# Performance work log

Measured on AMD Instinct MI355X. Metric: run time of the kernel, lower is better.

## Reference

```python
import jax, jax.numpy as jnp
import numpy as np

B, N, C, H = 4, 2048, 768, 12
D = C // H  # head_dim = 64


def setup_inputs() -> dict:
    key = jax.random.key(0)
    ks = jax.random.split(key, 16)
    s = 1.0 / np.sqrt(C)
    inp = {
        "x1": jax.random.normal(ks[0], (B, N, C), jnp.float32),
        "x2": jax.random.normal(ks[1], (B, N, C), jnp.float32),
        "mask_1": jax.random.uniform(ks[2], (B, N), jnp.float32),
        "mask_2": jax.random.uniform(ks[3], (B, N), jnp.float32),
        "Wq": jax.random.normal(ks[4], (C, C), jnp.float32) * s,
        "bq": jnp.zeros((C,), jnp.float32),
        "Wk": jax.random.normal(ks[5], (C, C), jnp.float32) * s,
        "bk": jnp.zeros((C,), jnp.float32),
        "Wv": jax.random.normal(ks[6], (C, C), jnp.float32) * s,
        "bv": jnp.zeros((C,), jnp.float32),
        "Wo": jax.random.normal(ks[7], (C, C), jnp.float32) * s,
        "bo": jnp.zeros((C,), jnp.float32),
        "temperature": jnp.asarray(1.0, jnp.float32),
        "ln_gamma": jnp.ones((C,), jnp.float32),
        "ln_beta": jnp.zeros((C,), jnp.float32),
    }
    return inp


def _layernorm(x, gamma, beta, eps=1e-5):
    mu = jnp.mean(x, axis=-1, keepdims=True)
    var = jnp.var(x, axis=-1, keepdims=True)
    return (x - mu) * jax.lax.rsqrt(var + eps) * gamma + beta


def reference(x1, x2, mask_1, mask_2, Wq, bq, Wk, bk, Wv, bv, Wo, bo,
              temperature, ln_gamma, ln_beta):
    # projections (nn.Linear: x @ W^T + b)
    q = (x1 @ Wq.T + bq).reshape(B, N, H, D).transpose(0, 2, 1, 3)  # [B,H,N,D]
    k = (x2 @ Wk.T + bk).reshape(B, N, H, D).transpose(0, 2, 1, 3)
    v = (x2 @ Wv.T + bv).reshape(B, N, H, D).transpose(0, 2, 1, 3)

    scores = jnp.einsum("bhnd,bhmd->bhnm", q, k) / jnp.sqrt(jnp.float32(D))
    # relative confidence bias: (mask_1[b,n] - mask_2[b,m]) / temperature
    rel = (mask_1[:, :, None] - mask_2[:, None, :]) / temperature  # [B,N,N]
    scores = scores + rel[:, None, :, :]

    attn = jax.nn.softmax(scores, axis=-1)  # dropout = identity (eval mode)
    out = jnp.einsum("bhnm,bhmd->bhnd", attn, v)
    out = out.transpose(0, 2, 1, 3).reshape(B, N, C)
    out = out @ Wo.T + bo
    return _layernorm(0.5 * x1 + out, ln_gamma, ln_beta)
```

## Files before the change

### kernel.cpp

```cpp
#include <hip/hip_runtime.h>
#include <stdint.h>

#define B_ 4
#define N_ 2048
#define C_ 768
#define H_ 12
#define D_ 64
#define NTOK 8192

typedef short bf16x8 __attribute__((ext_vector_type(8)));
typedef float f32x4 __attribute__((ext_vector_type(4)));
typedef float f32x16 __attribute__((ext_vector_type(16)));
typedef unsigned short ushort8 __attribute__((ext_vector_type(8)));
typedef unsigned short u16x4 __attribute__((ext_vector_type(4)));

__device__ __forceinline__ unsigned short f2bf(float f) {
  union { float f; unsigned u; } v; v.f = f;
  unsigned r = v.u + 0x7FFFu + ((v.u >> 16) & 1u);
  return (unsigned short)(r >> 16);
}

__device__ __forceinline__ void load_lds16(const void* g, void* lds_base) {
  __builtin_amdgcn_global_load_lds(
      (const __attribute__((address_space(1))) unsigned int*)g,
      (__attribute__((address_space(3))) unsigned int*)(uint32_t)(uintptr_t)lds_base,
      16, 0, 0);
}

__device__ __forceinline__ int key2slot(int key) {
  return ((key >> 5) << 5) | (((key >> 4) & 1) << 4) | (((key >> 2) & 1) << 3)
       | (((key >> 3) & 1) << 2) | (key & 3);
}

__device__ __forceinline__ bf16x8 pack8(const float* p) {
  union { unsigned u[4]; bf16x8 v; } r;
#pragma unroll
  for (int j=0;j<4;j++) {
    union { float f; unsigned u; } a, b;
    a.f = p[2*j]; b.f = p[2*j+1];
    r.u[j] = __builtin_amdgcn_perm(b.u + 0x8000u, a.u + 0x8000u, 0x07060302u);
  }
  return r.v;
}

__global__ __launch_bounds__(256) void cvt6(
    const float* s0, const float* s1, const float* s2, const float* s3,
    const float* s4, const float* s5,
    unsigned short* d0, unsigned short* d1, unsigned short* d2,
    unsigned short* d3, unsigned short* d4, unsigned short* d5,
    int n01, int n25)
{
  int y = blockIdx.y;
  const float* s = (y==0)?s0:(y==1)?s1:(y==2)?s2:(y==3)?s3:(y==4)?s4:s5;
  unsigned short* d = (y==0)?d0:(y==1)?d1:(y==2)?d2:(y==3)?d3:(y==4)?d4:d5;
  int n = (y<2) ? n01 : n25;
  int i = (blockIdx.x*256 + threadIdx.x)*8;
  if (i >= n) return;
  float4 f0 = *(const float4*)(s+i);
  float4 f1 = *(const float4*)(s+i+4);
  ushort8 o;
  o[0]=f2bf(f0.x); o[1]=f2bf(f0.y); o[2]=f2bf(f0.z); o[3]=f2bf(f0.w);
  o[4]=f2bf(f1.x); o[5]=f2bf(f1.y); o[6]=f2bf(f1.z); o[7]=f2bf(f1.w);
  *(ushort8*)(d+i) = o;
}

__device__ __forceinline__ void gemm_core(const unsigned short* A, const unsigned short* W,
                                          int rowBase, int colBase, f32x4 (&acc)[4][4],
                                          unsigned short* As, unsigned short* Bs)
{
  int tid = threadIdx.x, wave = tid>>6, lane = tid&63, quad = lane>>4, l16 = lane&15;
  int wm = wave>>1, wn = wave&1;
  for (int k0 = 0; k0 < 768; k0 += 32) {
    __syncthreads();
#pragma unroll
    for (int p = 0; p < 2; ++p) {
      int c = p*256 + wave*64 + lane;
      load_lds16(A + (size_t)(rowBase + (c>>2))*768 + k0 + (c&3)*8,
                 As + (size_t)(p*256 + wave*64)*8);
      load_lds16(W + (size_t)(colBase + (c>>2))*768 + k0 + (c&3)*8,
                 Bs + (size_t)(p*256 + wave*64)*8);
    }
    __syncthreads();
    bf16x8 af[4], bw[4];
#pragma unroll
    for (int i=0;i<4;i++) af[i] = *(const bf16x8*)(As + (wm*64 + i*16 + l16)*32 + quad*8);
#pragma unroll
    for (int j=0;j<4;j++) bw[j] = *(const bf16x8*)(Bs + (wn*64 + j*16 + l16)*32 + quad*8);
#pragma unroll
    for (int i=0;i<4;i++)
#pragma unroll
      for (int j=0;j<4;j++)
        acc[i][j] = __builtin_amdgcn_mfma_f32_16x16x32_bf16(af[i], bw[j], acc[i][j], 0,0,0);
  }
}

__global__ __launch_bounds__(256) void qkv_gemm(
    const unsigned short* xb1, const unsigned short* xb2,
    const unsigned short* Wq, const unsigned short* Wk, const unsigned short* Wv,
    const float* bq, const float* bk, const float* bv,
    unsigned short* Qb, unsigned short* Kb, unsigned short* Vb)
{
  __shared__ unsigned short As[128*32];
  __shared__ unsigned short Bs[128*32];
  int z = blockIdx.z;
  const unsigned short* A = (z==0) ? xb1 : xb2;
  const unsigned short* W = (z==0) ? Wq : (z==1) ? Wk : Wv;
  const float* bias       = (z==0) ? bq : (z==1) ? bk : bv;
  unsigned short* out     = (z==0) ? Qb : (z==1) ? Kb : Vb;
  int rowBase = blockIdx.x*128, colBase = blockIdx.y*128;
  int tid = threadIdx.x, wave = tid>>6, lane = tid&63, quad = lane>>4, l16 = lane&15;
  int wm = wave>>1, wn = wave&1;
  f32x4 acc[4][4] = {};
  gemm_core(A, W, rowBase, colBase, acc, As, Bs);
#pragma unroll
  for (int i=0;i<4;i++)
#pragma unroll
    for (int j=0;j<4;j++) {
      int col = colBase + wn*64 + j*16 + l16;
      float bv_ = bias[col];
      int h = col >> 6, d = col & 63;
#pragma unroll
      for (int r=0;r<4;r++) {
        int m = rowBase + wm*64 + i*16 + quad*4 + r;
        int b = m >> 11, n = m & 2047;
        out[(((size_t)b*H_ + h)*N_ + n)*D_ + d] = f2bf(acc[i][j][r] + bv_);
      }
    }
}

__global__ __launch_bounds__(256) void attn_kernel(
    const unsigned short* Qb, const unsigned short* Kb, const unsigned short* Vb,
    const float* mask2, const float* temp,
    unsigned short* Ob)
{
  __shared__ unsigned short Ks[64*64];
  __shared__ unsigned short Vt[64*64];
  __shared__ float m2s[64];
  const float LOG2E = 1.4426950408889634f;
  const float SCL = 0.125f * LOG2E;
  int qt = blockIdx.x, h = blockIdx.y, b = blockIdx.z;
  int tid = threadIdx.x, wave = tid>>6, lane = tid&63;
  int l32 = lane & 31, hl = lane >> 5;
  float invT = 1.0f / temp[0];
  size_t bh = (size_t)b*H_ + h;
  int qrow = qt*128 + wave*32 + l32;

  bf16x8 qf[4];
  const unsigned short* Qp = Qb + (bh*N_ + qrow)*D_;
#pragma unroll
  for (int i=0;i<4;i++) qf[i] = *(const bf16x8*)(Qp + i*16 + hl*8);

  int kp = tid & 31, vd0 = (tid >> 5) * 8;
  int s0 = key2slot(2*kp);
  int vch = (s0 >> 3) ^ (vd0 >> 3);

  float lrun = 0.f;
  f32x16 oacc0 = {}, oacc1 = {};

  for (int kt = 0; kt < N_/64; ++kt) {
    __syncthreads();
#pragma unroll
    for (int p=0;p<2;p++) {
      int idx = p*256 + tid;
      int key = idx >> 3, c = idx & 7;
      load_lds16(Kb + (bh*N_ + kt*64 + key)*D_ + (c ^ (key & 7))*8,
                 Ks + (size_t)(p*256 + wave*64)*8);
    }
    {
      const unsigned short* vsrc = Vb + (bh*N_ + kt*64 + 2*kp)*D_ + vd0;
      bf16x8 v0 = *(const bf16x8*)(vsrc);
      bf16x8 v1 = *(const bf16x8*)(vsrc + D_);
#pragma unroll
      for (int jj=0;jj<8;jj++) {
        unsigned val = (unsigned)(unsigned short)v0[jj]
                     | ((unsigned)(unsigned short)v1[jj] << 16);
        *(unsigned*)(Vt + (vd0+jj)*64 + vch*8 + (s0 & 7)) = val;
      }
    }
    if (tid < 64) m2s[tid] = (-mask2[b*N_ + kt*64 + tid] * invT - 8.0f) * LOG2E;
    __syncthreads();

#pragma unroll
    for (int sub=0; sub<2; ++sub) {
      f32x16 sa = {};
#pragma unroll
      for (int i=0;i<4;i++) {
        int ch = (2*i + hl) ^ (l32 & 7);
        bf16x8 kf = *(const bf16x8*)(Ks + (sub*32 + l32)*64 + ch*8);
        sa = __builtin_amdgcn_mfma_f32_32x32x16_bf16(kf, qf[i], sa, 0,0,0);
      }
      float pv[16];
#pragma unroll
      for (int g=0; g<4; ++g) {
        float4 mv = *(const float4*)(m2s + sub*32 + g*8 + hl*4);
#pragma unroll
        for (int q=0;q<4;q++)
          pv[g*4+q] = __builtin_amdgcn_exp2f(sa[g*4+q]*SCL + ((const float*)&mv)[q]);
      }
      bf16x8 pf0 = pack8(pv);
      bf16x8 pf1 = pack8(pv+8);
#pragma unroll
      for (int kc=0;kc<2;kc++) {
        bf16x8 pf = kc ? pf1 : pf0;
        int c = sub*4 + kc*2 + hl;
        {
          int d = l32;
          bf16x8 vf = *(const bf16x8*)(Vt + d*64 + (c ^ ((d>>3)&7))*8);
          oacc0 = __builtin_amdgcn_mfma_f32_32x32x16_bf16(vf, pf, oacc0, 0,0,0);
        }
        {
          int d = 32 + l32;
          bf16x8 vf = *(const bf16x8*)(Vt + d*64 + (c ^ ((d>>3)&7))*8);
          oacc1 = __builtin_amdgcn_mfma_f32_32x32x16_bf16(vf, pf, oacc1, 0,0,0);
        }
      }
      float rs = 0.f;
#pragma unroll
      for (int r=0;r<16;r++) rs += pv[r];
      lrun += rs;
    }
  }

  lrun += __shfl_xor(lrun, 32);
  float rinv = 1.0f / lrun;
  size_t obase = ((size_t)b*N_ + qrow)*C_ + h*D_;
#pragma unroll
  for (int dh=0; dh<2; ++dh)
#pragma unroll
    for (int g=0; g<4; ++g) {
      int d = dh*32 + g*8 + hl*4;
      u16x4 o;
#pragma unroll
      for (int q=0;q<4;q++) {
        float val = (dh==0 ? oacc0[g*4+q] : oacc1[g*4+q]) * rinv;
        o[q] = f2bf(val);
      }
      *(u16x4*)(Ob + obase + d) = o;
    }
}

__global__ __launch_bounds__(256) void out_gemm(
    const unsigned short* Ob, const unsigned short* Wo, const float* bo,
    const float* x1, float* Z)
{
  __shared__ unsigned short As[128*32];
  __shared__ unsigned short Bs[128*32];
  int rowBase = blockIdx.x*128, colBase = blockIdx.y*128;
  int tid = threadIdx.x, wave = tid>>6, lane = tid&63, quad = lane>>4, l16 = lane&15;
  int wm = wave>>1, wn = wave&1;
  f32x4 acc[4][4] = {};
  gemm_core(Ob, Wo, rowBase, colBase, acc, As, Bs);
#pragma unroll
  for (int i=0;i<4;i++)
#pragma unroll
    for (int j=0;j<4;j++) {
      int col = colBase + wn*64 + j*16 + l16;
      float bv_ = bo[col];
#pragma unroll
      for (int r=0;r<4;r++) {
        size_t m = rowBase + wm*64 + i*16 + quad*4 + r;
        Z[m*768 + col] = acc[i][j][r] + bv_ + 0.5f*x1[m*768 + col];
      }
    }
}

__global__ __launch_bounds__(256) void ln_kernel(const float* Z, const float* gam,
                                                 const float* bet, float* out)
{
  size_t row = blockIdx.x;
  int t = threadIdx.x;
  const float* z = Z + row*768;
  float v0 = z[t], v1 = z[t+256], v2 = z[t+512];
  float s = v0+v1+v2;
  float ss = v0*v0 + v1*v1 + v2*v2;
#pragma unroll
  for (int off=1; off<64; off<<=1) { s += __shfl_xor(s, off); ss += __shfl_xor(ss, off); }
  __shared__ float red[8];
  int wave = t>>6, lane = t&63;
  if (lane==0) { red[wave] = s; red[4+wave] = ss; }
  __syncthreads();
  float S = red[0]+red[1]+red[2]+red[3];
  float SS = red[4]+red[5]+red[6]+red[7];
  float mean = S * (1.0f/768.0f);
  float var = SS * (1.0f/768.0f) - mean*mean;
  float rstd = rsqrtf(var + 1e-5f);
  float* o = out + row*768;
  o[t]     = (v0-mean)*rstd*gam[t]     + bet[t];
  o[t+256] = (v1-mean)*rstd*gam[t+256] + bet[t+256];
  o[t+512] = (v2-mean)*rstd*gam[t+512] + bet[t+512];
}

extern "C" void kernel_launch(void* const* d_in, const int* in_sizes, int n_in,
                              void* d_out, int out_size, void* d_ws, size_t ws_size,
                              hipStream_t stream)
{
  const float* x1    = (const float*)d_in[0];
  const float* x2    = (const float*)d_in[1];
  const float* mask2 = (const float*)d_in[3];
  const float* Wq    = (const float*)d_in[4];
  const float* bq    = (const float*)d_in[5];
  const float* Wk    = (const float*)d_in[6];
  const float* bk    = (const float*)d_in[7];
  const float* Wv    = (const float*)d_in[8];
  const float* bv    = (const float*)d_in[9];
  const float* Wo    = (const float*)d_in[10];
  const float* bo    = (const float*)d_in[11];
  const float* temp  = (const float*)d_in[12];
  const float* gam   = (const float*)d_in[13];
  const float* bet   = (const float*)d_in[14];

  char* ws = (char*)d_ws;
  size_t off = 0;
  auto alloc = [&](size_t bytes) { void* p = ws + off; off += (bytes + 255) & ~255ull; return p; };
  const size_t XB = (size_t)NTOK * C_ * 2;
  const size_t WB = (size_t)C_ * C_ * 2;
  unsigned short* xb1 = (unsigned short*)alloc(XB);
  unsigned short* xb2 = (unsigned short*)alloc(XB);
  unsigned short* Wqb = (unsigned short*)alloc(WB);
  unsigned short* Wkb = (unsigned short*)alloc(WB);
  unsigned short* Wvb = (unsigned short*)alloc(WB);
  unsigned short* Wob = (unsigned short*)alloc(WB);
  unsigned short* Qb  = (unsigned short*)alloc(XB);
  unsigned short* Kb  = (unsigned short*)alloc(XB);
  unsigned short* Vb  = (unsigned short*)alloc(XB);
  unsigned short* Ob  = (unsigned short*)alloc(XB);
  float* Z = (float*)xb1;

  cvt6<<<dim3(3072, 6), 256, 0, stream>>>(x1, x2, Wq, Wk, Wv, Wo,
                                          xb1, xb2, Wqb, Wkb, Wvb, Wob,
                                          NTOK*C_, C_*C_);
  qkv_gemm<<<dim3(64, 6, 3), 256, 0, stream>>>(xb1, xb2, Wqb, Wkb, Wvb,
                                               bq, bk, bv, Qb, Kb, Vb);
  attn_kernel<<<dim3(16, 12, 4), 256, 0, stream>>>(Qb, Kb, Vb, mask2, temp, Ob);
  out_gemm<<<dim3(64, 6), 256, 0, stream>>>(Ob, Wob, bo, x1, Z);
  ln_kernel<<<dim3(8192), 256, 0, stream>>>(Z, gam, bet, (float*)d_out);
}
```

Before: 288.3 us.

## Pre-transpose V in QKV GEMM, double-buffer K/V loads, precompute mask row

The QKV GEMM now writes V transposed (head-dim major, with keys permuted into slot order) so the attention kernel can load V tiles into LDS through direct global-to-LDS loads instead of an in-register transpose. K and V tiles are double-buffered, so the loads for the next tile are issued while the current tile is being computed, with one barrier per iteration. The full mask_2 bias row is precomputed into LDS once per block. The grid is flattened and remapped so blocks of the same batch-head share an XCD, which should improve L2 reuse of K/V. In exchange LDS use grows and the V layout is now coupled to the key2slot permutation.

Result: no change. 292.8 us (+1.6%).

```diff
diff --git a/kernel.cpp b/kernel.cpp
--- a/kernel.cpp
+++ b/kernel.cpp
@@ -112,87 +112,117 @@
   int wm = wave>>1, wn = wave&1;
   f32x4 acc[4][4] = {};
   gemm_core(A, W, rowBase, colBase, acc, As, Bs);
-#pragma unroll
-  for (int i=0;i<4;i++)
-#pragma unroll
-    for (int j=0;j<4;j++) {
-      int col = colBase + wn*64 + j*16 + l16;
-      float bv_ = bias[col];
-      int h = col >> 6, d = col & 63;
-#pragma unroll
-      for (int r=0;r<4;r++) {
-        int m = rowBase + wm*64 + i*16 + quad*4 + r;
-        int b = m >> 11, n = m & 2047;
-        out[(((size_t)b*H_ + h)*N_ + n)*D_ + d] = f2bf(acc[i][j][r] + bv_);
-      }
-    }
+  if (z == 2) {
+#pragma unroll
+    for (int i=0;i<4;i++)
+#pragma unroll
+      for (int j=0;j<4;j++) {
+        int col = colBase + wn*64 + j*16 + l16;
+        float bv_ = bias[col];
+        int h = col >> 6, d = col & 63;
+        int m0 = rowBase + wm*64 + i*16 + quad*4;
+        int b = m0 >> 11, n0 = m0 & 2047;
+        int nslot = (n0 & ~63) | key2slot(n0 & 63);
+        u16x4 o;
+#pragma unroll
+        for (int r=0;r<4;r++) o[r] = f2bf(acc[i][j][r] + bv_);
+        *(u16x4*)(out + ((size_t)(b*H_ + h)*D_ + d)*N_ + nslot) = o;
+      }
+  } else {
+#pragma unroll
+    for (int i=0;i<4;i++)
+#pragma unroll
+      for (int j=0;j<4;j++) {
+        int col = colBase + wn*64 + j*16 + l16;
+        float bv_ = bias[col];
+        int h = col >> 6, d = col & 63;
+#pragma unroll
+        for (int r=0;r<4;r++) {
+          int m = rowBase + wm*64 + i*16 + quad*4 + r;
+          int b = m >> 11, n = m & 2047;
+          out[(((size_t)b*H_ + h)*N_ + n)*D_ + d] = f2bf(acc[i][j][r] + bv_);
+        }
+      }
+  }
+}
+
+__device__ __forceinline__ void attn_stage(const unsigned short* Kb, const unsigned short* Vtg,
+                                           size_t bh, int kt, int tid, int wave,
+                                           unsigned short* KsBuf, unsigned short* VsBuf)
+{
+#pragma unroll
+  for (int p=0;p<2;p++) {
+    int idx = p*256 + tid;
+    int key = idx >> 3, c = idx & 7;
+    load_lds16(Kb + (bh*N_ + (size_t)kt*64 + key)*D_ + (c ^ (key & 7))*8,
+               KsBuf + (size_t)(p*256 + wave*64)*8);
+  }
+#pragma unroll
+  for (int p=0;p<2;p++) {
+    int idx = p*256 + tid;
+    int d = idx >> 3, c = idx & 7;
+    load_lds16(Vtg + (bh*D_ + d)*(size_t)N_ + kt*64 + (c ^ (d & 7))*8,
+               VsBuf + (size_t)(p*256 + wave*64)*8);
+  }
 }
 
 __global__ __launch_bounds__(256) void attn_kernel(
-    const unsigned short* Qb, const unsigned short* Kb, const unsigned short* Vb,
+    const unsigned short* Qb, const unsigned short* Kb, const unsigned short* Vtg,
     const float* mask2, const float* temp,
     unsigned short* Ob)
 {
-  __shared__ unsigned short Ks[64*64];
-  __shared__ unsigned short Vt[64*64];
-  __shared__ float m2s[64];
+  __shared__ unsigned short Ks[2][64*64];
+  __shared__ unsigned short Vs[2][64*64];
+  __shared__ float m2x[N_];
   const float LOG2E = 1.4426950408889634f;
   const float SCL = 0.125f * LOG2E;
-  int qt = blockIdx.x, h = blockIdx.y, b = blockIdx.z;
+  int bx = blockIdx.x;
+  int xcd = bx & 7, slot = bx >> 3;
+  int bh_i = xcd*6 + (slot >> 4);
+  int qt = slot & 15;
+  int b = bh_i / H_, h = bh_i - b*H_; (void)h;
   int tid = threadIdx.x, wave = tid>>6, lane = tid&63;
   int l32 = lane & 31, hl = lane >> 5;
   float invT = 1.0f / temp[0];
-  size_t bh = (size_t)b*H_ + h;
+  size_t bh = (size_t)bh_i;
   int qrow = qt*128 + wave*32 + l32;
+
+#pragma unroll
+  for (int r=0;r<8;r++) {
+    int i = r*256 + tid;
+    m2x[i] = (-mask2[b*N_ + i]*invT - 8.0f) * LOG2E;
+  }
 
   bf16x8 qf[4];
   const unsigned short* Qp = Qb + (bh*N_ + qrow)*D_;
 #pragma unroll
   for (int i=0;i<4;i++) qf[i] = *(const bf16x8*)(Qp + i*16 + hl*8);
 
-  int kp = tid & 31, vd0 = (tid >> 5) * 8;
-  int s0 = key2slot(2*kp);
-  int vch = (s0 >> 3) ^ (vd0 >> 3);
-
   float lrun = 0.f;
   f32x16 oacc0 = {}, oacc1 = {};
 
+  attn_stage(Kb, Vtg, bh, 0, tid, wave, Ks[0], Vs[0]);
+  __syncthreads();
+
   for (int kt = 0; kt < N_/64; ++kt) {
-    __syncthreads();
-#pragma unroll
-    for (int p=0;p<2;p++) {
-      int idx = p*256 + tid;
-      int key = idx >> 3, c = idx & 7;
-      load_lds16(Kb + (bh*N_ + kt*64 + key)*D_ + (c ^ (key & 7))*8,
-                 Ks + (size_t)(p*256 + wave*64)*8);
-    }
-    {
-      const unsigned short* vsrc = Vb + (bh*N_ + kt*64 + 2*kp)*D_ + vd0;
-      bf16x8 v0 = *(const bf16x8*)(vsrc);
-      bf16x8 v1 = *(const bf16x8*)(vsrc + D_);
-#pragma unroll
-      for (int jj=0;jj<8;jj++) {
-        unsigned val = (unsigned)(unsigned short)v0[jj]
-                     | ((unsigned)(unsigned short)v1[jj] << 16);
-        *(unsigned*)(Vt + (vd0+jj)*64 + vch*8 + (s0 & 7)) = val;
-      }
-    }
-    if (tid < 64) m2s[tid] = (-mask2[b*N_ + kt*64 + tid] * invT - 8.0f) * LOG2E;
-    __syncthreads();
-
+    int cur = kt & 1;
+    if (kt+1 < N_/64)
+      attn_stage(Kb, Vtg, bh, kt+1, tid, wave, Ks[cur^1], Vs[cur^1]);
+    const unsigned short* Kc = Ks[cur];
+    const unsigned short* Vc = Vs[cur];
 #pragma unroll
     for (int sub=0; sub<2; ++sub) {
       f32x16 sa = {};
 #pragma unroll
       for (int i=0;i<4;i++) {
         int ch = (2*i + hl) ^ (l32 & 7);
-        bf16x8 kf = *(const bf16x8*)(Ks + (sub*32 + l32)*64 + ch*8);
+        bf16x8 kf = *(const bf16x8*)(Kc + (sub*32 + l32)*64 + ch*8);
         sa = __builtin_amdgcn_mfma_f32_32x32x16_bf16(kf, qf[i], sa, 0,0,0);
       }
       float pv[16];
 #pragma unroll
       for (int g=0; g<4; ++g) {
-        float4 mv = *(const float4*)(m2s + sub*32 + g*8 + hl*4);
+        float4 mv = *(const float4*)(m2x + kt*64 + sub*32 + g*8 + hl*4);
 #pragma unroll
         for (int q=0;q<4;q++)
           pv[g*4+q] = __builtin_amdgcn_exp2f(sa[g*4+q]*SCL + ((const float*)&mv)[q]);
@@ -202,15 +232,15 @@
 #pragma unroll
       for (int kc=0;kc<2;kc++) {
         bf16x8 pf = kc ? pf1 : pf0;
-        int c = sub*4 + kc*2 + hl;
+        int cc = sub*4 + kc*2 + hl;
         {
           int d = l32;
-          bf16x8 vf = *(const bf16x8*)(Vt + d*64 + (c ^ ((d>>3)&7))*8);
+          bf16x8 vf = *(const bf16x8*)(Vc + d*64 + (cc ^ (d&7))*8);
           oacc0 = __builtin_amdgcn_mfma_f32_32x32x16_bf16(vf, pf, oacc0, 0,0,0);
         }
         {
           int d = 32 + l32;
-          bf16x8 vf = *(const bf16x8*)(Vt + d*64 + (c ^ ((d>>3)&7))*8);
+          bf16x8 vf = *(const bf16x8*)(Vc + d*64 + (cc ^ (d&7))*8);
           oacc1 = __builtin_amdgcn_mfma_f32_32x32x16_bf16(vf, pf, oacc1, 0,0,0);
         }
       }
@@ -219,6 +249,7 @@
       for (int r=0;r<16;r++) rs += pv[r];
       lrun += rs;
     }
+    __syncthreads();
   }
 
   lrun += __shfl_xor(lrun, 32);
@@ -331,7 +362,7 @@
                                           NTOK*C_, C_*C_);
   qkv_gemm<<<dim3(64, 6, 3), 256, 0, stream>>>(xb1, xb2, Wqb, Wkb, Wvb,
                                                bq, bk, bv, Qb, Kb, Vb);
-  attn_kernel<<<dim3(16, 12, 4), 256, 0, stream>>>(Qb, Kb, Vb, mask2, temp, Ob);
+  attn_kernel<<<dim3(768), 256, 0, stream>>>(Qb, Kb, Vb, mask2, temp, Ob);
   out_gemm<<<dim3(64, 6), 256, 0, stream>>>(Ob, Wob, bo, x1, Z);
   ln_kernel<<<dim3(8192), 256, 0, stream>>>(Z, gam, bet, (float*)d_out);
 }
```
